# Kernel optimization log

Hardware: AMD Instinct MI355X
Metric: run time of the kernel (lower is better)

The kernel has to match this reference:

```python
import jax, jax.numpy as jnp
import numpy as np

TARGET = 560   # target_size
EPS = 1e-8


def setup_inputs() -> dict:
    key = jax.random.key(0)
    k1, k2, k3, k4 = jax.random.split(key, 4)
    B, K, D, C, N = 2, 1600, 1024, 256, 32
    feats = jax.random.normal(k1, (B, K, D), dtype=jnp.float32)
    embedding = jax.random.normal(k2, (C, D), dtype=jnp.float32)
    # valid boxes: x_min,y_min in [0, 400), side in [16, 160) => min_box_size satisfied, in-bounds
    xy_min = jax.random.randint(k3, (B, N, 2), 0, TARGET - 160)
    wh = jax.random.randint(k4, (B, N, 2), 16, 160)
    xy_max = jnp.minimum(xy_min + wh, TARGET)
    boxes = jnp.concatenate([xy_min, xy_max], axis=-1).astype(jnp.int32)  # (B,N,4) = x_min,y_min,x_max,y_max
    return {"feats": feats, "embedding": embedding, "boxes": boxes}


def reference(feats, embedding, boxes):
    # feats: (B,K,D) patch features, embedding: (C,D) class prototypes, boxes: (B,N,4) int
    B, K, D = feats.shape
    C = embedding.shape[0]
    P = int(np.sqrt(K))  # patch_2d_size

    # --- get_cosim_mini_batch (normalize=True), fused as a single GEMM + norm ---
    dot = jnp.einsum('bkd,cd->bck', feats, embedding)          # (B,C,K)
    feats_norm = jnp.linalg.norm(feats, axis=-1)               # (B,K)
    emb_norm = jnp.linalg.norm(embedding, axis=-1)             # (C,)
    cosim = dot / (feats_norm[:, None, :] * emb_norm[None, :, None] + EPS)
    cosim = cosim.reshape(B, C, P, P)
    cosim = jax.image.resize(cosim, (B, C, TARGET, TARGET), method='bicubic')  # (B,C,560,560)
    # single scale -> stack().mean(0) is identity

    # --- box mean pooling: cosim[b,:,y_min:y_max-1, x_min:x_max-1].mean((1,2)) via masks ---
    x_min, y_min, x_max, y_max = boxes[..., 0], boxes[..., 1], boxes[..., 2], boxes[..., 3]
    r = jnp.arange(TARGET)
    my = ((r[None, None, :] >= y_min[..., None]) & (r[None, None, :] <= y_max[..., None] - 2)).astype(cosim.dtype)  # (B,N,H)
    mx = ((r[None, None, :] >= x_min[..., None]) & (r[None, None, :] <= x_max[..., None] - 2)).astype(cosim.dtype)  # (B,N,W)
    counts = my.sum(-1) * mx.sum(-1)                           # (B,N)
    pooled = jnp.einsum('bnh,bnw,bchw->bnc', my, mx, cosim)    # (B,N,C)
    box_sim = pooled / counts[..., None]
    return box_sim.reshape(-1, C)
```

## Files before the change

kernel.cpp:

```cpp
#include <hip/hip_runtime.h>
#include <hip/hip_bf16.h>
#include <math.h>

#define TGT 560
#define B_ 2
#define K_ 1600
#define D_ 1024
#define C_ 256
#define N_ 32
#define P_ 40
#define KC_ 32
#define KCHUNK 50

#define OFF_IFN ((size_t)0)
#define OFF_IEN (OFF_IFN + (size_t)B_ * K_)
#define OFF_BOXW (OFF_IEN + (size_t)C_)
#define OFF_G   ((size_t)16384)

__global__ __launch_bounds__(256) void kA(const float* __restrict__ feats,
                                          const float* __restrict__ emb,
                                          const int* __restrict__ boxes,
                                          float* __restrict__ ws) {
    __shared__ float shm[80];
    const int r = blockIdx.x;
    const int t = threadIdx.x;
    if (r < B_ * K_ + C_) {
        const float* src;
        float* dst;
        if (r < B_ * K_) { src = feats + (size_t)r * D_; dst = ws + OFF_IFN + r; }
        else             { src = emb + (size_t)(r - B_ * K_) * D_; dst = ws + OFF_IEN + (r - B_ * K_); }
        float4 v = ((const float4*)src)[t];
        float s = v.x * v.x + v.y * v.y + v.z * v.z + v.w * v.w;
        #pragma unroll
        for (int off = 32; off > 0; off >>= 1) s += __shfl_down(s, off, 64);
        if ((t & 63) == 0) shm[t >> 6] = s;
        __syncthreads();
        if (t == 0) {
            float tot = shm[0] + shm[1] + shm[2] + shm[3];
            *dst = 1.0f / sqrtf(tot);
        }
    } else {
        const int bn = r - (B_ * K_ + C_);
        ((float4*)(ws + OFF_G + (size_t)bn * D_))[t] = make_float4(0.f, 0.f, 0.f, 0.f);
        if (t < 80) shm[t] = 0.f;
        __syncthreads();
        const int* bx = boxes + bn * 4;
        const int xmin = bx[0], ymin = bx[1], xmax = bx[2], ymax = bx[3];
        const float invcnt = 1.0f / ((float)(ymax - 1 - ymin) * (float)(xmax - 1 - xmin));
        const int axis = t >> 7;
        const int rr = t & 127;
        const int lo = (axis ? xmin : ymin);
        const int hi = (axis ? xmax : ymax) - 2;
        for (int h = lo + rr; h <= hi; h += 128) {
            float sf = ((float)h + 0.5f) * (1.0f / 14.0f) - 0.5f;
            int jf = (int)floorf(sf);
            float w[4];
            float norm = 0.f;
            #pragma unroll
            for (int dj = -1; dj <= 2; ++dj) {
                int j = jf + dj;
                float x = fabsf(sf - (float)j);
                float wv = ((1.5f * x - 2.5f) * x) * x + 1.f;
                if (x >= 1.f) wv = ((-0.5f * x + 2.5f) * x - 4.f) * x + 2.f;
                if (x >= 2.f) wv = 0.f;
                if (j < 0 || j >= P_) wv = 0.f;
                w[dj + 1] = wv;
                norm += wv;
            }
            float inv = 1.0f / norm;
            #pragma unroll
            for (int dj = 0; dj < 4; ++dj) {
                int j = jf - 1 + dj;
                if (w[dj] != 0.f) atomicAdd(&shm[axis * P_ + j], w[dj] * inv);
            }
        }
        __syncthreads();
        if (t < 80) {
            float val = shm[t];
            if (t < P_) val *= invcnt;
            ws[OFF_BOXW + (size_t)bn * 80 + t] = val;
        }
    }
}

__global__ __launch_bounds__(256) void kB(const float* __restrict__ feats,
                                          const float* __restrict__ ws,
                                          float* __restrict__ g) {
    __shared__ float sw[N_ * 80];
    __shared__ float vlds[KCHUNK * N_];
    const int bid = blockIdx.x;
    const int b = bid >> 7;
    const int rest = bid & 127;
    const int kc = rest >> 2;
    const int dt = rest & 3;
    const int t = threadIdx.x;
    const int k0 = kc * KCHUNK;

    for (int i = t; i < N_ * 80; i += 256)
        sw[i] = ws[OFF_BOXW + (size_t)b * N_ * 80 + i];
    __syncthreads();
    const float* ifn = ws + OFF_IFN + (size_t)b * K_;
    for (int i = t; i < KCHUNK * N_; i += 256) {
        int kk = i >> 5, n = i & 31;
        int k = k0 + kk;
        int pq = k / P_;
        int q = k - pq * P_;
        vlds[kk * N_ + n] = sw[n * 80 + pq] * sw[n * 80 + P_ + q] * ifn[k];
    }
    __syncthreads();

    float acc[N_];
    #pragma unroll
    for (int n = 0; n < N_; ++n) acc[n] = 0.f;

    const float* fp = feats + ((size_t)b * K_ + k0) * D_ + dt * 256 + t;
    #pragma unroll
    for (int gi = 0; gi < 5; ++gi) {
        float f[10];
        #pragma unroll
        for (int u = 0; u < 10; ++u) f[u] = fp[(size_t)(gi * 10 + u) * D_];
        #pragma unroll
        for (int u = 0; u < 10; ++u) {
            const float4* vp = (const float4*)&vlds[(gi * 10 + u) * N_];
            #pragma unroll
            for (int j = 0; j < 8; ++j) {
                float4 v4 = vp[j];
                acc[4 * j + 0] = fmaf(v4.x, f[u], acc[4 * j + 0]);
                acc[4 * j + 1] = fmaf(v4.y, f[u], acc[4 * j + 1]);
                acc[4 * j + 2] = fmaf(v4.z, f[u], acc[4 * j + 2]);
                acc[4 * j + 3] = fmaf(v4.w, f[u], acc[4 * j + 3]);
            }
        }
    }
    float* o = g + (size_t)b * N_ * D_ + dt * 256 + t;
    #pragma unroll
    for (int n = 0; n < N_; ++n) atomicAdd(&o[(size_t)n * D_], acc[n]);
}

__global__ __launch_bounds__(256) void kC(const float* __restrict__ emb,
                                          const float* __restrict__ g,
                                          const float* __restrict__ ien,
                                          float* __restrict__ out) {
    __shared__ float4 g4sh[4][D_ / 4];
    __shared__ float part[16][4];
    const int bid = blockIdx.x;
    const int bng = bid >> 4;
    const int ct  = bid & 15;
    const int t = threadIdx.x;
    const int lane = t & 63;
    const int wv = t >> 6;

    #pragma unroll
    for (int bn = 0; bn < 4; ++bn)
        g4sh[bn][t] = ((const float4*)(g + (size_t)(bng * 4 + bn) * D_))[t];
    __syncthreads();

    float p[4][4];
    #pragma unroll
    for (int cc = 0; cc < 4; ++cc)
        #pragma unroll
        for (int bn = 0; bn < 4; ++bn) p[cc][bn] = 0.f;

    #pragma unroll
    for (int i = 0; i < 4; ++i) {
        float4 gv[4];
        #pragma unroll
        for (int bn = 0; bn < 4; ++bn) gv[bn] = g4sh[bn][lane + 64 * i];
        #pragma unroll
        for (int cc = 0; cc < 4; ++cc) {
            const int c = ct * 16 + wv * 4 + cc;
            float4 e = ((const float4*)(emb + (size_t)c * D_))[lane + 64 * i];
            #pragma unroll
            for (int bn = 0; bn < 4; ++bn)
                p[cc][bn] += e.x * gv[bn].x + e.y * gv[bn].y + e.z * gv[bn].z + e.w * gv[bn].w;
        }
    }
    #pragma unroll
    for (int cc = 0; cc < 4; ++cc) {
        #pragma unroll
        for (int bn = 0; bn < 4; ++bn) {
            float v = p[cc][bn];
            #pragma unroll
            for (int off = 32; off > 0; off >>= 1) v += __shfl_down(v, off, 64);
            if (lane == 0) part[wv * 4 + cc][bn] = v;
        }
    }
    __syncthreads();
    if (t < 64) {
        const int c = t >> 2, bn = t & 3;
        out[(size_t)(bng * 4 + bn) * C_ + ct * 16 + c] = part[c][bn] * ien[ct * 16 + c];
    }
}

extern "C" void kernel_launch(void* const* d_in, const int* in_sizes, int n_in,
                              void* d_out, int out_size, void* d_ws, size_t ws_size,
                              hipStream_t stream) {
    const float* feats = (const float*)d_in[0];
    const float* emb   = (const float*)d_in[1];
    const int*   boxes = (const int*)d_in[2];
    float* out = (float*)d_out;
    float* ws  = (float*)d_ws;

    kA<<<B_ * K_ + C_ + B_ * N_, 256, 0, stream>>>(feats, emb, boxes, ws);
    kB<<<B_ * KC_ * 4, 256, 0, stream>>>(feats, ws, ws + OFF_G);
    kC<<<256, 256, 0, stream>>>(emb, ws + OFF_G, ws + OFF_IEN, out);
}
```

Before: 90.78 us.

## Fuse three kernels into one cooperative kernel with grid syncs and deterministic partial reduction

Merges the norm/box-weight, feature-projection and embedding-dot kernels into a single cooperative launch of 256 blocks separated by grid.sync. Norms are now computed one row per wave in a grid-stride loop. The global atomicAdd accumulation of g is replaced by per-chunk partial buffers followed by a separate reduction phase. This removes two kernel launches and the atomics, at the cost of extra workspace traffic for the partials, three grid-wide barriers, and fewer blocks working on the norm phase.

```diff
diff --git a/kernel.cpp b/kernel.cpp
--- a/kernel.cpp
+++ b/kernel.cpp
@@ -1,6 +1,8 @@
 #include <hip/hip_runtime.h>
-#include <hip/hip_bf16.h>
+#include <hip/hip_cooperative_groups.h>
 #include <math.h>
+
+namespace cg = cooperative_groups;
 
 #define TGT 560
 #define B_ 2
@@ -16,179 +18,193 @@
 #define OFF_IEN (OFF_IFN + (size_t)B_ * K_)
 #define OFF_BOXW (OFF_IEN + (size_t)C_)
 #define OFF_G   ((size_t)16384)
-
-__global__ __launch_bounds__(256) void kA(const float* __restrict__ feats,
-                                          const float* __restrict__ emb,
-                                          const int* __restrict__ boxes,
-                                          float* __restrict__ ws) {
-    __shared__ float shm[80];
-    const int r = blockIdx.x;
-    const int t = threadIdx.x;
-    if (r < B_ * K_ + C_) {
-        const float* src;
-        float* dst;
-        if (r < B_ * K_) { src = feats + (size_t)r * D_; dst = ws + OFF_IFN + r; }
-        else             { src = emb + (size_t)(r - B_ * K_) * D_; dst = ws + OFF_IEN + (r - B_ * K_); }
-        float4 v = ((const float4*)src)[t];
-        float s = v.x * v.x + v.y * v.y + v.z * v.z + v.w * v.w;
-        #pragma unroll
-        for (int off = 32; off > 0; off >>= 1) s += __shfl_down(s, off, 64);
-        if ((t & 63) == 0) shm[t >> 6] = s;
-        __syncthreads();
-        if (t == 0) {
-            float tot = shm[0] + shm[1] + shm[2] + shm[3];
-            *dst = 1.0f / sqrtf(tot);
-        }
-    } else {
-        const int bn = r - (B_ * K_ + C_);
-        ((float4*)(ws + OFF_G + (size_t)bn * D_))[t] = make_float4(0.f, 0.f, 0.f, 0.f);
-        if (t < 80) shm[t] = 0.f;
-        __syncthreads();
-        const int* bx = boxes + bn * 4;
-        const int xmin = bx[0], ymin = bx[1], xmax = bx[2], ymax = bx[3];
-        const float invcnt = 1.0f / ((float)(ymax - 1 - ymin) * (float)(xmax - 1 - xmin));
-        const int axis = t >> 7;
-        const int rr = t & 127;
-        const int lo = (axis ? xmin : ymin);
-        const int hi = (axis ? xmax : ymax) - 2;
-        for (int h = lo + rr; h <= hi; h += 128) {
-            float sf = ((float)h + 0.5f) * (1.0f / 14.0f) - 0.5f;
-            int jf = (int)floorf(sf);
-            float w[4];
-            float norm = 0.f;
-            #pragma unroll
-            for (int dj = -1; dj <= 2; ++dj) {
-                int j = jf + dj;
-                float x = fabsf(sf - (float)j);
-                float wv = ((1.5f * x - 2.5f) * x) * x + 1.f;
-                if (x >= 1.f) wv = ((-0.5f * x + 2.5f) * x - 4.f) * x + 2.f;
-                if (x >= 2.f) wv = 0.f;
-                if (j < 0 || j >= P_) wv = 0.f;
-                w[dj + 1] = wv;
-                norm += wv;
-            }
-            float inv = 1.0f / norm;
-            #pragma unroll
-            for (int dj = 0; dj < 4; ++dj) {
-                int j = jf - 1 + dj;
-                if (w[dj] != 0.f) atomicAdd(&shm[axis * P_ + j], w[dj] * inv);
-            }
-        }
-        __syncthreads();
-        if (t < 80) {
-            float val = shm[t];
-            if (t < P_) val *= invcnt;
-            ws[OFF_BOXW + (size_t)bn * 80 + t] = val;
-        }
-    }
-}
-
-__global__ __launch_bounds__(256) void kB(const float* __restrict__ feats,
-                                          const float* __restrict__ ws,
-                                          float* __restrict__ g) {
-    __shared__ float sw[N_ * 80];
-    __shared__ float vlds[KCHUNK * N_];
+#define OFF_GP  (OFF_G + (size_t)B_ * N_ * D_)
+
+__global__ __launch_bounds__(256) void fused(const float* __restrict__ feats,
+                                             const float* __restrict__ emb,
+                                             const int* __restrict__ boxes,
+                                             float* __restrict__ ws,
+                                             float* __restrict__ out) {
+    __shared__ __align__(16) float smem[4224];
     const int bid = blockIdx.x;
-    const int b = bid >> 7;
-    const int rest = bid & 127;
-    const int kc = rest >> 2;
-    const int dt = rest & 3;
-    const int t = threadIdx.x;
-    const int k0 = kc * KCHUNK;
-
-    for (int i = t; i < N_ * 80; i += 256)
-        sw[i] = ws[OFF_BOXW + (size_t)b * N_ * 80 + i];
-    __syncthreads();
-    const float* ifn = ws + OFF_IFN + (size_t)b * K_;
-    for (int i = t; i < KCHUNK * N_; i += 256) {
-        int kk = i >> 5, n = i & 31;
-        int k = k0 + kk;
-        int pq = k / P_;
-        int q = k - pq * P_;
-        vlds[kk * N_ + n] = sw[n * 80 + pq] * sw[n * 80 + P_ + q] * ifn[k];
-    }
-    __syncthreads();
-
-    float acc[N_];
-    #pragma unroll
-    for (int n = 0; n < N_; ++n) acc[n] = 0.f;
-
-    const float* fp = feats + ((size_t)b * K_ + k0) * D_ + dt * 256 + t;
-    #pragma unroll
-    for (int gi = 0; gi < 5; ++gi) {
-        float f[10];
-        #pragma unroll
-        for (int u = 0; u < 10; ++u) f[u] = fp[(size_t)(gi * 10 + u) * D_];
-        #pragma unroll
-        for (int u = 0; u < 10; ++u) {
-            const float4* vp = (const float4*)&vlds[(gi * 10 + u) * N_];
-            #pragma unroll
-            for (int j = 0; j < 8; ++j) {
-                float4 v4 = vp[j];
-                acc[4 * j + 0] = fmaf(v4.x, f[u], acc[4 * j + 0]);
-                acc[4 * j + 1] = fmaf(v4.y, f[u], acc[4 * j + 1]);
-                acc[4 * j + 2] = fmaf(v4.z, f[u], acc[4 * j + 2]);
-                acc[4 * j + 3] = fmaf(v4.w, f[u], acc[4 * j + 3]);
-            }
-        }
-    }
-    float* o = g + (size_t)b * N_ * D_ + dt * 256 + t;
-    #pragma unroll
-    for (int n = 0; n < N_; ++n) atomicAdd(&o[(size_t)n * D_], acc[n]);
-}
-
-__global__ __launch_bounds__(256) void kC(const float* __restrict__ emb,
-                                          const float* __restrict__ g,
-                                          const float* __restrict__ ien,
-                                          float* __restrict__ out) {
-    __shared__ float4 g4sh[4][D_ / 4];
-    __shared__ float part[16][4];
-    const int bid = blockIdx.x;
-    const int bng = bid >> 4;
-    const int ct  = bid & 15;
     const int t = threadIdx.x;
     const int lane = t & 63;
     const int wv = t >> 6;
-
-    #pragma unroll
-    for (int bn = 0; bn < 4; ++bn)
-        g4sh[bn][t] = ((const float4*)(g + (size_t)(bng * 4 + bn) * D_))[t];
-    __syncthreads();
-
-    float p[4][4];
-    #pragma unroll
-    for (int cc = 0; cc < 4; ++cc)
-        #pragma unroll
-        for (int bn = 0; bn < 4; ++bn) p[cc][bn] = 0.f;
-
-    #pragma unroll
-    for (int i = 0; i < 4; ++i) {
-        float4 gv[4];
-        #pragma unroll
-        for (int bn = 0; bn < 4; ++bn) gv[bn] = g4sh[bn][lane + 64 * i];
+    cg::grid_group grid = cg::this_grid();
+
+    {
+        const int gw = bid * 4 + wv;
+        for (int r = gw; r < B_ * K_ + C_; r += 1024) {
+            const float* src;
+            float* dst;
+            if (r < B_ * K_) { src = feats + (size_t)r * D_; dst = ws + OFF_IFN + r; }
+            else             { src = emb + (size_t)(r - B_ * K_) * D_; dst = ws + OFF_IEN + (r - B_ * K_); }
+            const float4* p4 = (const float4*)src;
+            float s = 0.f;
+            #pragma unroll
+            for (int i = 0; i < 4; ++i) {
+                float4 v = p4[lane + 64 * i];
+                s += v.x * v.x + v.y * v.y + v.z * v.z + v.w * v.w;
+            }
+            #pragma unroll
+            for (int off = 32; off > 0; off >>= 1) s += __shfl_down(s, off, 64);
+            if (lane == 0) *dst = 1.0f / sqrtf(s);
+        }
+        if (bid < 16) {
+            for (int i = t; i < 320; i += 256) smem[i] = 0.f;
+            __syncthreads();
+            const int bn = bid * 4 + wv;
+            const int* bx = boxes + bn * 4;
+            const int xmin = bx[0], ymin = bx[1], xmax = bx[2], ymax = bx[3];
+            float* wsl = smem + wv * 80;
+            #pragma unroll
+            for (int axis = 0; axis < 2; ++axis) {
+                const int lo = axis ? xmin : ymin;
+                const int hi = (axis ? xmax : ymax) - 2;
+                for (int h = lo + lane; h <= hi; h += 64) {
+                    float sf = ((float)h + 0.5f) * (1.0f / 14.0f) - 0.5f;
+                    int jf = (int)floorf(sf);
+                    float w[4];
+                    float norm = 0.f;
+                    #pragma unroll
+                    for (int dj = -1; dj <= 2; ++dj) {
+                        int j = jf + dj;
+                        float x = fabsf(sf - (float)j);
+                        float wvv = ((1.5f * x - 2.5f) * x) * x + 1.f;
+                        if (x >= 1.f) wvv = ((-0.5f * x + 2.5f) * x - 4.f) * x + 2.f;
+                        if (x >= 2.f) wvv = 0.f;
+                        if (j < 0 || j >= P_) wvv = 0.f;
+                        w[dj + 1] = wvv;
+                        norm += wvv;
+                    }
+                    float inv = 1.0f / norm;
+                    #pragma unroll
+                    for (int dj = 0; dj < 4; ++dj) {
+                        int j = jf - 1 + dj;
+                        if (w[dj] != 0.f) atomicAdd(&wsl[axis * P_ + j], w[dj] * inv);
+                    }
+                }
+            }
+            __syncthreads();
+            const float invcnt = 1.0f / ((float)(ymax - 1 - ymin) * (float)(xmax - 1 - xmin));
+            for (int i = lane; i < 80; i += 64) {
+                float val = smem[wv * 80 + i];
+                if (i < P_) val *= invcnt;
+                ws[OFF_BOXW + (size_t)bn * 80 + i] = val;
+            }
+        }
+    }
+    grid.sync();
+
+    {
+        const int b = bid >> 7;
+        const int rest = bid & 127;
+        const int kc = rest >> 2;
+        const int dt = rest & 3;
+        const int k0 = kc * KCHUNK;
+        float* sw = smem;
+        float* vlds = smem + N_ * 80;
+
+        for (int i = t; i < N_ * 80; i += 256)
+            sw[i] = ws[OFF_BOXW + (size_t)b * N_ * 80 + i];
+        __syncthreads();
+        const float* ifn = ws + OFF_IFN + (size_t)b * K_;
+        for (int i = t; i < KCHUNK * N_; i += 256) {
+            int kk = i >> 5, n = i & 31;
+            int k = k0 + kk;
+            int pq = k / P_;
+            int q = k - pq * P_;
+            vlds[kk * N_ + n] = sw[n * 80 + pq] * sw[n * 80 + P_ + q] * ifn[k];
+        }
+        __syncthreads();
+
+        float acc[N_];
+        #pragma unroll
+        for (int n = 0; n < N_; ++n) acc[n] = 0.f;
+
+        const float* fp = feats + ((size_t)b * K_ + k0) * D_ + dt * 256 + t;
+        #pragma unroll
+        for (int gi = 0; gi < 5; ++gi) {
+            float f[10];
+            #pragma unroll
+            for (int u = 0; u < 10; ++u) f[u] = fp[(size_t)(gi * 10 + u) * D_];
+            #pragma unroll
+            for (int u = 0; u < 10; ++u) {
+                const float4* vp = (const float4*)&vlds[(gi * 10 + u) * N_];
+                #pragma unroll
+                for (int j = 0; j < 8; ++j) {
+                    float4 v4 = vp[j];
+                    acc[4 * j + 0] = fmaf(v4.x, f[u], acc[4 * j + 0]);
+                    acc[4 * j + 1] = fmaf(v4.y, f[u], acc[4 * j + 1]);
+                    acc[4 * j + 2] = fmaf(v4.z, f[u], acc[4 * j + 2]);
+                    acc[4 * j + 3] = fmaf(v4.w, f[u], acc[4 * j + 3]);
+                }
+            }
+        }
+        float* gp = ws + OFF_GP + ((((size_t)b * KC_ + kc) * 4 + dt) * N_) * 256 + t;
+        #pragma unroll
+        for (int n = 0; n < N_; ++n) gp[(size_t)n * 256] = acc[n];
+    }
+    grid.sync();
+
+    {
+        const int e = bid * 256 + t;
+        const int bn = e >> 10, d = e & 1023;
+        const int b2 = bn >> 5, n2 = bn & 31, dt2 = d >> 8, dd = d & 255;
+        const float* src = ws + OFF_GP + ((size_t)((b2 * 128 + dt2) * 32 + n2)) * 256 + dd;
+        float s = 0.f;
+        #pragma unroll
+        for (int kc = 0; kc < KC_; ++kc) s += src[(size_t)kc * 32768];
+        ws[OFF_G + e] = s;
+    }
+    grid.sync();
+
+    {
+        const int bng = bid >> 4;
+        const int ct = bid & 15;
+        float4* g4sh = (float4*)smem;
+        float* part = smem + 4096;
+        const float* g = ws + OFF_G;
+        #pragma unroll
+        for (int bn = 0; bn < 4; ++bn)
+            g4sh[bn * 256 + t] = ((const float4*)(g + (size_t)(bng * 4 + bn) * D_))[t];
+        __syncthreads();
+
+        float p[4][4];
+        #pragma unroll
+        for (int cc = 0; cc < 4; ++cc)
+            #pragma unroll
+            for (int bn = 0; bn < 4; ++bn) p[cc][bn] = 0.f;
+
+        #pragma unroll
+        for (int i = 0; i < 4; ++i) {
+            float4 gv[4];
+            #pragma unroll
+            for (int bn = 0; bn < 4; ++bn) gv[bn] = g4sh[bn * 256 + lane + 64 * i];
+            #pragma unroll
+            for (int cc = 0; cc < 4; ++cc) {
+                const int c = ct * 16 + wv * 4 + cc;
+                float4 e4 = ((const float4*)(emb + (size_t)c * D_))[lane + 64 * i];
+                #pragma unroll
+                for (int bn = 0; bn < 4; ++bn)
+                    p[cc][bn] += e4.x * gv[bn].x + e4.y * gv[bn].y + e4.z * gv[bn].z + e4.w * gv[bn].w;
+            }
+        }
         #pragma unroll
         for (int cc = 0; cc < 4; ++cc) {
-            const int c = ct * 16 + wv * 4 + cc;
-            float4 e = ((const float4*)(emb + (size_t)c * D_))[lane + 64 * i];
-            #pragma unroll
-            for (int bn = 0; bn < 4; ++bn)
-                p[cc][bn] += e.x * gv[bn].x + e.y * gv[bn].y + e.z * gv[bn].z + e.w * gv[bn].w;
-        }
-    }
-    #pragma unroll
-    for (int cc = 0; cc < 4; ++cc) {
-        #pragma unroll
-        for (int bn = 0; bn < 4; ++bn) {
-            float v = p[cc][bn];
-            #pragma unroll
-            for (int off = 32; off > 0; off >>= 1) v += __shfl_down(v, off, 64);
-            if (lane == 0) part[wv * 4 + cc][bn] = v;
-        }
-    }
-    __syncthreads();
-    if (t < 64) {
-        const int c = t >> 2, bn = t & 3;
-        out[(size_t)(bng * 4 + bn) * C_ + ct * 16 + c] = part[c][bn] * ien[ct * 16 + c];
+            #pragma unroll
+            for (int bn = 0; bn < 4; ++bn) {
+                float v = p[cc][bn];
+                #pragma unroll
+                for (int off = 32; off > 0; off >>= 1) v += __shfl_down(v, off, 64);
+                if (lane == 0) part[(wv * 4 + cc) * 4 + bn] = v;
+            }
+        }
+        __syncthreads();
+        if (t < 64) {
+            const int c = t >> 2, bn = t & 3;
+            out[(size_t)(bng * 4 + bn) * C_ + ct * 16 + c] = part[c * 4 + bn] * ws[OFF_IEN + ct * 16 + c];
+        }
     }
 }
 
@@ -201,7 +217,6 @@
     float* out = (float*)d_out;
     float* ws  = (float*)d_ws;
 
-    kA<<<B_ * K_ + C_ + B_ * N_, 256, 0, stream>>>(feats, emb, boxes, ws);
-    kB<<<B_ * KC_ * 4, 256, 0, stream>>>(feats, ws, ws + OFF_G);
-    kC<<<256, 256, 0, stream>>>(emb, ws + OFF_G, ws + OFF_IEN, out);
+    void* args[] = {(void*)&feats, (void*)&emb, (void*)&boxes, (void*)&ws, (void*)&out};
+    hipLaunchCooperativeKernel(fused, dim3(256), dim3(256), args, 0, stream);
 }
```

Measured after the change: 187.1 us. 2.06x slower.
